# Performance work log

Hardware: AMD Instinct MI355X
Metric: run time of the kernel (lower is better)

The kernel has to match this reference:

```python
import jax, jax.numpy as jnp
import numpy as np

B, C, L = 4, 512, 2048
CI = 512          # inter_channels (must equal num_heads*head_dim)
H, D = 8, 64      # num_heads, head_dim = C // H
EPS = 1e-5        # BatchNorm1d eps


def setup_inputs() -> dict:
    key = jax.random.key(0)
    ks = jax.random.split(key, 9)
    s_in = 1.0 / np.sqrt(C)
    s_ci = 1.0 / np.sqrt(CI)
    return {
        "x": jax.random.normal(ks[0], (B, C, L), dtype=jnp.float32),
        "g_w": jax.random.uniform(ks[1], (CI, C), jnp.float32, -s_in, s_in),
        "g_b": jax.random.uniform(ks[2], (CI,), jnp.float32, -s_in, s_in),
        "theta_w": jax.random.uniform(ks[3], (CI, C), jnp.float32, -s_in, s_in),
        "theta_b": jax.random.uniform(ks[4], (CI,), jnp.float32, -s_in, s_in),
        "phi_w": jax.random.uniform(ks[5], (CI, C), jnp.float32, -s_in, s_in),
        "phi_b": jax.random.uniform(ks[6], (CI,), jnp.float32, -s_in, s_in),
        "w_w": jax.random.uniform(ks[7], (C, CI), jnp.float32, -s_ci, s_ci),
        "w_b": jax.random.uniform(ks[8], (C,), jnp.float32, -s_ci, s_ci),
        # BN affine params (torch inits them to 0, which zeroes the output;
        # use random values so the reference output / grads are non-trivial)
        "bn_gamma": jax.random.normal(jax.random.fold_in(key, 10), (C,), jnp.float32),
        "bn_beta": jax.random.normal(jax.random.fold_in(key, 11), (C,), jnp.float32),
    }


def _conv1x1(w, b, x):
    # x: [B, Cin, L], w: [Cout, Cin] -> [B, Cout, L]
    return jnp.einsum("oc,bcl->bol", w, x) + b[None, :, None]


def reference(x, g_w, g_b, theta_w, theta_b, phi_w, phi_b, w_w, w_b, bn_gamma, bn_beta):
    b, _, l = x.shape
    # 1x1 conv projections, split into heads: [B, H, D, L]
    g_x = _conv1x1(g_w, g_b, x).reshape(b, H, D, l).transpose(0, 1, 3, 2)      # [B,H,L,D]
    theta_x = _conv1x1(theta_w, theta_b, x).reshape(b, H, D, l).transpose(0, 1, 3, 2)  # [B,H,L,D]
    phi_x = _conv1x1(phi_w, phi_b, x).reshape(b, H, D, l)                       # [B,H,D,L]

    scale = 1.0 / jnp.sqrt(jnp.asarray(D, dtype=x.dtype))
    scores = jnp.einsum("bhqd,bhdk->bhqk", theta_x, phi_x) * scale  # [B,H,L,L]
    attn = jax.nn.softmax(scores, axis=-1)
    y = jnp.einsum("bhqk,bhkd->bhqd", attn, g_x)                    # [B,H,L,D]
    y = y.transpose(0, 1, 3, 2).reshape(b, CI, l)                   # [B,CI,L]

    # W: 1x1 conv + BatchNorm1d (training mode, biased batch stats)
    wy = _conv1x1(w_w, w_b, y)                                      # [B,C,L]
    mean = jnp.mean(wy, axis=(0, 2), keepdims=True)
    var = jnp.mean((wy - mean) ** 2, axis=(0, 2), keepdims=True)
    wy_hat = (wy - mean) * jax.lax.rsqrt(var + EPS)
    return wy_hat * bn_gamma[None, :, None] + bn_beta[None, :, None]
```

## Files before the change

### kernel.cpp

```cpp
#include <hip/hip_runtime.h>

constexpr int Bn = 4, Cn = 512, Ln = 2048, CIn = 512, Hn = 8, Dn = 64;
constexpr int COn = 3 * CIn;

typedef unsigned short u16;
typedef unsigned int u32;
typedef __attribute__((ext_vector_type(8))) short bfrag;
typedef __attribute__((ext_vector_type(4))) float facc;

#define SCF 0.180336879f

__device__ __forceinline__ facc mfma16(bfrag a, bfrag b, facc c) {
  return __builtin_amdgcn_mfma_f32_16x16x32_bf16(a, b, c, 0, 0, 0);
}

__device__ __forceinline__ void async16(const void* g, void* l) {
  __builtin_amdgcn_global_load_lds((const __attribute__((address_space(1))) void*)g,
                                   (__attribute__((address_space(3))) void*)l, 16, 0, 0);
}

__device__ __forceinline__ u16 f2bf(float x) {
  union { float f; u32 u; } v; v.f = x;
  u32 r = v.u + 0x7FFFu + ((v.u >> 16) & 1u);
  return (u16)(r >> 16);
}

__device__ __forceinline__ u16 f2bf_fast(float x) {
  union { float f; u32 u; } v; v.f = x;
  return (u16)((v.u + 0x8000u) >> 16);
}

__device__ __forceinline__ u32 pkbf(float lof, float hif) {
  union { float f; u32 u; } a, b; a.f = lof; b.f = hif;
  return __builtin_amdgcn_perm(b.u + 0x8000u, a.u + 0x8000u, 0x07060302u);
}

__device__ __forceinline__ bfrag fr8(const u16* base, int row, int gi) {
  return *(const bfrag*)&base[row * 64 + ((gi ^ (row & 7)) * 8)];
}

__global__ void k_wconv(const float* __restrict__ gw, const float* __restrict__ tw,
                        const float* __restrict__ pw, const float* __restrict__ ww,
                        u16* __restrict__ Wcat, u16* __restrict__ Ww,
                        float* __restrict__ stats) {
  int i = blockIdx.x * 256 + threadIdx.x;
  if (i < CIn * Cn) {
    Wcat[i]                = f2bf(tw[i] * SCF);
    Wcat[CIn * Cn + i]     = f2bf(pw[i]);
    Wcat[2 * CIn * Cn + i] = f2bf(gw[i]);
    Ww[i]                  = f2bf(ww[i]);
  }
  if (i < 2 * Cn) stats[i] = 0.f;
}

__global__ void k_xpose(const float* __restrict__ x, u16* __restrict__ xT) {
  __shared__ float tile[32][33];
  int b = blockIdx.z;
  int l0 = blockIdx.x * 32, c0 = blockIdx.y * 32;
  int tx = threadIdx.x & 31, ty = threadIdx.x >> 5;
  const float* xb = x + (size_t)b * Cn * Ln;
  for (int k = 0; k < 4; k++)
    tile[ty + k * 8][tx] = xb[(size_t)(c0 + ty + k * 8) * Ln + l0 + tx];
  __syncthreads();
  u16* xtb = xT + (size_t)b * Ln * Cn;
  int cc = (threadIdx.x & 15) * 2, r0 = threadIdx.x >> 4;
  for (int k = 0; k < 2; k++) {
    int ll = r0 + k * 16;
    u32 pk = pkbf(tile[cc][ll], tile[cc + 1][ll]);
    *(u32*)&xtb[(size_t)(l0 + ll) * Cn + c0 + cc] = pk;
  }
}

__device__ __forceinline__ void stage128x32(const u16* g, int K, int k0, u16* lds,
                                            int w, int l) {
  int gsw = ((l & 3) ^ ((l >> 3) & 3)) * 8;
  for (int jj = 0; jj < 2; jj++) {
    int j = w * 2 + jj;
    const u16* ga = g + (size_t)(j * 16 + (l >> 2)) * K + k0 + gsw;
    async16(ga, (char*)lds + j * 1024 + l * 16);
  }
}

__device__ __forceinline__ void gemm_core(const u16* A, const u16* Bt, int K,
                                          u16* As, u16* Bs, facc acc[4][4],
                                          int w, int l) {
  int quad = l >> 4, lo = l & 15;
  int mw = (w >> 1) * 64, nw = (w & 1) * 64;
  int rsw = (lo >> 1) & 3;
  for (int k0 = 0; k0 < K; k0 += 32) {
    stage128x32(A, K, k0, As, w, l);
    stage128x32(Bt, K, k0, Bs, w, l);
    __syncthreads();
    bfrag af[4], bfv[4];
    for (int mi = 0; mi < 4; mi++)
      af[mi] = *(const bfrag*)&As[(mw + mi * 16 + lo) * 32 + ((quad ^ rsw) * 8)];
    for (int ni = 0; ni < 4; ni++)
      bfv[ni] = *(const bfrag*)&Bs[(nw + ni * 16 + lo) * 32 + ((quad ^ rsw) * 8)];
    for (int mi = 0; mi < 4; mi++)
      for (int ni = 0; ni < 4; ni++)
        acc[mi][ni] = mfma16(af[mi], bfv[ni], acc[mi][ni]);
    __syncthreads();
  }
}

__global__ __launch_bounds__(256) void k_proj(
    const u16* __restrict__ Wcat, const u16* __restrict__ xT,
    const float* __restrict__ tb, const float* __restrict__ pb,
    const float* __restrict__ gb, u16* __restrict__ Q, u16* __restrict__ Kb,
    u16* __restrict__ Vt) {
  __shared__ __align__(16) u16 As[128 * 32];
  __shared__ __align__(16) u16 Bs[128 * 32];
  int w = threadIdx.x >> 6, l = threadIdx.x & 63;
  int quad = l >> 4, lo = l & 15;
  int m0 = blockIdx.y * 128, n0 = blockIdx.x * 128, b = blockIdx.z;
  facc acc[4][4] = {};
  gemm_core(Wcat + (size_t)m0 * Cn, xT + ((size_t)b * Ln + n0) * Cn, Cn, As, Bs, acc, w, l);
  int mw = (w >> 1) * 64, nw = (w & 1) * 64;
  int chunk = m0 >> 9;
  for (int mi = 0; mi < 4; mi++) {
    int mo = (m0 + mw + mi * 16) & 511;
    int hh = mo >> 6;
    int db = (mo & 63) + quad * 4;
    int bi = mo + quad * 4;
    if (chunk < 2) {
      const float* bias = (chunk == 0) ? tb : pb;
      float bs = (chunk == 0) ? SCF : 1.0f;
      u16* dst0 = ((chunk == 0) ? Q : Kb) + (size_t)(b * Hn + hh) * Ln * 64 + db;
      float b0 = bias[bi] * bs, b1 = bias[bi + 1] * bs;
      float b2 = bias[bi + 2] * bs, b3 = bias[bi + 3] * bs;
      for (int ni = 0; ni < 4; ni++) {
        int lcol = n0 + nw + ni * 16 + lo;
        facc a = acc[mi][ni];
        uint2 pk;
        pk.x = pkbf(a[0] + b0, a[1] + b1);
        pk.y = pkbf(a[2] + b2, a[3] + b3);
        *(uint2*)(dst0 + (size_t)lcol * 64) = pk;
      }
    } else {
      for (int ni = 0; ni < 4; ni++) {
        int lcol = n0 + nw + ni * 16 + lo;
        facc a = acc[mi][ni];
        for (int r = 0; r < 4; r++)
          Vt[((size_t)(b * Hn + hh) * Dn + db + r) * Ln + lcol] = f2bf_fast(a[r] + gb[bi + r]);
      }
    }
  }
}

__global__ __launch_bounds__(256, 2) void k_attn(
    const u16* __restrict__ Q, const u16* __restrict__ Kb,
    const u16* __restrict__ Vt, u16* __restrict__ yT) {
  __shared__ __align__(16) u16 lds[24576];
  u16* Ks = lds;
  u16* Vs = lds + 8192;
  u16* QPs = lds + 16384;
  int w = threadIdx.x >> 6, l = threadIdx.x & 63;
  int quad = l >> 4, lo = l & 15;
  int q0 = blockIdx.x * 128, h = blockIdx.y, b = blockIdx.z;
  size_t bh = (size_t)b * Hn + h;
  const u16* Qg = Q + bh * Ln * 64;
  const u16* Kg = Kb + bh * Ln * 64;
  const u16* Vg = Vt + bh * (size_t)Dn * Ln;

  int rin = l >> 3;
  int gg = ((l & 7) ^ rin) * 8;

  for (int jj = 0; jj < 4; jj++) {
    int j = w * 4 + jj;
    async16(Qg + (size_t)(q0 + j * 8 + rin) * 64 + gg, (char*)QPs + j * 1024 + l * 16);
  }
  for (int jj = 0; jj < 2; jj++) {
    int j = w * 2 + jj;
    async16(Kg + (size_t)(j * 8 + rin) * 64 + gg, (char*)Ks + j * 1024 + l * 16);
    async16(Vg + (size_t)(j * 8 + rin) * Ln + gg, (char*)Vs + j * 1024 + l * 16);
  }
  __syncthreads();
  bfrag qf[2][2];
  for (int s = 0; s < 2; s++)
    for (int c = 0; c < 2; c++)
      qf[s][c] = fr8(QPs, w * 32 + s * 16 + lo, c * 4 + quad);

  facc o[2][4] = {};
  float l_i[2] = {0.f, 0.f};

  for (int t = 0; t < 32; t++) {
    const u16* Kc = Ks + (t & 1) * 4096;
    const u16* Vc = Vs + (t & 1) * 4096;
    if (t < 31) {
      int nb = (~t & 1) * 4096;
      int kbase = (t + 1) * 64;
      for (int jj = 0; jj < 2; jj++) {
        int j = w * 2 + jj;
        async16(Kg + (size_t)(kbase + j * 8 + rin) * 64 + gg,
                (char*)(Ks + nb) + j * 1024 + l * 16);
        async16(Vg + (size_t)(j * 8 + rin) * Ln + kbase + gg,
                (char*)(Vs + nb) + j * 1024 + l * 16);
      }
    }
    for (int ni = 0; ni < 4; ni++) {
      bfrag kf0 = fr8(Kc, ni * 16 + lo, quad);
      bfrag kf1 = fr8(Kc, ni * 16 + lo, 4 + quad);
      for (int s = 0; s < 2; s++) {
        facc z = {};
        facc stv = mfma16(kf1, qf[s][1], mfma16(kf0, qf[s][0], z));
        float p0 = __builtin_amdgcn_exp2f(stv[0]);
        float p1 = __builtin_amdgcn_exp2f(stv[1]);
        float p2 = __builtin_amdgcn_exp2f(stv[2]);
        float p3 = __builtin_amdgcn_exp2f(stv[3]);
        l_i[s] += (p0 + p1) + (p2 + p3);
        int row = w * 32 + s * 16 + lo;
        uint2 pk;
        pk.x = pkbf(p0, p1);
        pk.y = pkbf(p2, p3);
        int gi = ni * 2 + (quad >> 1);
        *(uint2*)&QPs[row * 64 + ((gi ^ (row & 7)) * 8) + (quad & 1) * 4] = pk;
      }
    }
    bfrag pb2[2][2];
    for (int s = 0; s < 2; s++)
      for (int c = 0; c < 2; c++)
        pb2[s][c] = fr8(QPs, w * 32 + s * 16 + lo, c * 4 + quad);
    for (int mi = 0; mi < 4; mi++) {
      bfrag vf0 = fr8(Vc, mi * 16 + lo, quad);
      bfrag vf1 = fr8(Vc, mi * 16 + lo, 4 + quad);
      for (int s = 0; s < 2; s++)
        o[s][mi] = mfma16(vf1, pb2[s][1], mfma16(vf0, pb2[s][0], o[s][mi]));
    }
    __syncthreads();
  }
  for (int s = 0; s < 2; s++) {
    float lt = l_i[s];
    lt += __shfl_xor(lt, 16);
    lt += __shfl_xor(lt, 32);
    float inv = 1.0f / lt;
    int q = q0 + w * 32 + s * 16 + lo;
    u16* dst = yT + ((size_t)b * Ln + q) * CIn + h * 64;
    for (int mi = 0; mi < 4; mi++) {
      uint2 pk;
      pk.x = pkbf(o[s][mi][0] * inv, o[s][mi][1] * inv);
      pk.y = pkbf(o[s][mi][2] * inv, o[s][mi][3] * inv);
      *(uint2*)(dst + mi * 16 + quad * 4) = pk;
    }
  }
}

__global__ __launch_bounds__(256) void k_wgemm(
    const u16* __restrict__ Ww, const u16* __restrict__ yT,
    const float* __restrict__ wb, u16* __restrict__ wy,
    float* __restrict__ stats) {
  __shared__ __align__(16) u16 As[128 * 32];
  __shared__ __align__(16) u16 Bs[128 * 32];
  int w = threadIdx.x >> 6, l = threadIdx.x & 63;
  int quad = l >> 4, lo = l & 15;
  int m0 = blockIdx.y * 128, n0 = blockIdx.x * 128, b = blockIdx.z;
  facc acc[4][4] = {};
  gemm_core(Ww + (size_t)m0 * CIn, yT + ((size_t)b * Ln + n0) * CIn, CIn, As, Bs, acc, w, l);
  int mw = (w >> 1) * 64, nw = (w & 1) * 64;
  for (int mi = 0; mi < 4; mi++) {
    int cb = m0 + mw + mi * 16 + quad * 4;
    for (int r = 0; r < 4; r++) {
      float bias = wb[cb + r];
      float s = 0.f, q = 0.f;
      for (int ni = 0; ni < 4; ni++) {
        float v = acc[mi][ni][r] + bias;
        wy[((size_t)b * Cn + cb + r) * Ln + n0 + nw + ni * 16 + lo] = f2bf_fast(v);
        s += v; q += v * v;
      }
      for (int mask = 1; mask < 16; mask <<= 1) {
        s += __shfl_xor(s, mask);
        q += __shfl_xor(q, mask);
      }
      if (lo == 0) {
        atomicAdd(&stats[cb + r], s);
        atomicAdd(&stats[Cn + cb + r], q);
      }
    }
  }
}

__global__ void k_bn(const u16* __restrict__ wy, const float* __restrict__ stats,
                     const float* __restrict__ gam, const float* __restrict__ bet,
                     float* __restrict__ out) {
  int i = blockIdx.x * 256 + threadIdx.x;
  size_t idx = (size_t)i * 8;
  int c = (int)((idx >> 11) & (Cn - 1));
  const float invN = 1.f / (Bn * Ln);
  float mean = stats[c] * invN;
  float var = stats[Cn + c] * invN - mean * mean;
  float scl = gam[c] * rsqrtf(var + 1e-5f);
  float sh = bet[c] - mean * scl;
  uint4 v = *(const uint4*)(wy + idx);
  float4 o0, o1;
  o0.x = __uint_as_float((v.x & 0xFFFFu) << 16) * scl + sh;
  o0.y = __uint_as_float((v.x & 0xFFFF0000u)) * scl + sh;
  o0.z = __uint_as_float((v.y & 0xFFFFu) << 16) * scl + sh;
  o0.w = __uint_as_float((v.y & 0xFFFF0000u)) * scl + sh;
  o1.x = __uint_as_float((v.z & 0xFFFFu) << 16) * scl + sh;
  o1.y = __uint_as_float((v.z & 0xFFFF0000u)) * scl + sh;
  o1.z = __uint_as_float((v.w & 0xFFFFu) << 16) * scl + sh;
  o1.w = __uint_as_float((v.w & 0xFFFF0000u)) * scl + sh;
  *(float4*)(out + idx) = o0;
  *(float4*)(out + idx + 4) = o1;
}

extern "C" void kernel_launch(void* const* d_in, const int* in_sizes, int n_in,
                              void* d_out, int out_size, void* d_ws, size_t ws_size,
                              hipStream_t stream) {
  const float* x   = (const float*)d_in[0];
  const float* g_w = (const float*)d_in[1];
  const float* g_b = (const float*)d_in[2];
  const float* t_w = (const float*)d_in[3];
  const float* t_b = (const float*)d_in[4];
  const float* p_w = (const float*)d_in[5];
  const float* p_b = (const float*)d_in[6];
  const float* w_w = (const float*)d_in[7];
  const float* w_b = (const float*)d_in[8];
  const float* gam = (const float*)d_in[9];
  const float* bet = (const float*)d_in[10];
  float* out = (float*)d_out;

  char* ws = (char*)d_ws;
  size_t off = 0;
  auto alloc = [&](size_t bytes) {
    char* p = ws + off; off += (bytes + 255) & ~(size_t)255; return p;
  };
  u16*  xT   = (u16*)alloc((size_t)Bn * Ln * Cn * 2);
  u16*  Wcat = (u16*)alloc((size_t)COn * Cn * 2);
  u16*  Ww   = (u16*)alloc((size_t)Cn * CIn * 2);
  u16*  Qb   = (u16*)alloc((size_t)Bn * Hn * Ln * Dn * 2);
  u16*  Kb   = (u16*)alloc((size_t)Bn * Hn * Ln * Dn * 2);
  u16*  Vt   = (u16*)alloc((size_t)Bn * Hn * Dn * Ln * 2);
  u16*  yT   = (u16*)alloc((size_t)Bn * Ln * CIn * 2);
  u16*  wy   = (u16*)alloc((size_t)Bn * Cn * Ln * 2);
  float* st  = (float*)alloc(2 * Cn * 4);
  if (ws_size < off) return;

  k_wconv<<<dim3(1024), 256, 0, stream>>>(g_w, t_w, p_w, w_w, Wcat, Ww, st);
  k_xpose<<<dim3(64, 16, 4), 256, 0, stream>>>(x, xT);
  k_proj<<<dim3(16, 12, 4), 256, 0, stream>>>(Wcat, xT, t_b, p_b, g_b, Qb, Kb, Vt);
  k_attn<<<dim3(16, 8, 4), 256, 0, stream>>>(Qb, Kb, Vt, yT);
  k_wgemm<<<dim3(16, 4, 4), 256, 0, stream>>>(Ww, yT, w_b, wy, st);
  k_bn<<<dim3(2048), 256, 0, stream>>>(wy, st, gam, bet, out);
}
```

Before: 204.3 us.

## Split attention over key halves, shrink W-GEMM tiles, merge prep kernels

The attention kernel now splits the key/value range into two halves per query tile. Each half writes unnormalised partial outputs and row sums, and a new combine kernel adds them and normalises into yT. This doubles the attention grid and shortens each block's serial key loop. The W-conv GEMM moves to 64-row tiles to double its block count, and the weight-conversion and transpose kernels are merged into one launch. The cost is an extra kernel, a round-trip of the partial outputs through memory, and bf16 rounding of the partials before they are combined.

Measured after the change: 195.5 us. 1.04x faster.

```diff
diff --git a/kernel.cpp b/kernel.cpp
--- a/kernel.cpp
+++ b/kernel.cpp
@@ -35,27 +35,31 @@
   return __builtin_amdgcn_perm(b.u + 0x8000u, a.u + 0x8000u, 0x07060302u);
 }
 
+__device__ __forceinline__ float bflo(u32 u) { return __uint_as_float(u << 16); }
+__device__ __forceinline__ float bfhi(u32 u) { return __uint_as_float(u & 0xFFFF0000u); }
+
 __device__ __forceinline__ bfrag fr8(const u16* base, int row, int gi) {
   return *(const bfrag*)&base[row * 64 + ((gi ^ (row & 7)) * 8)];
 }
 
-__global__ void k_wconv(const float* __restrict__ gw, const float* __restrict__ tw,
-                        const float* __restrict__ pw, const float* __restrict__ ww,
-                        u16* __restrict__ Wcat, u16* __restrict__ Ww,
-                        float* __restrict__ stats) {
-  int i = blockIdx.x * 256 + threadIdx.x;
-  if (i < CIn * Cn) {
-    Wcat[i]                = f2bf(tw[i] * SCF);
-    Wcat[CIn * Cn + i]     = f2bf(pw[i]);
-    Wcat[2 * CIn * Cn + i] = f2bf(gw[i]);
-    Ww[i]                  = f2bf(ww[i]);
-  }
-  if (i < 2 * Cn) stats[i] = 0.f;
-}
-
-__global__ void k_xpose(const float* __restrict__ x, u16* __restrict__ xT) {
+__global__ void k_misc(const float* __restrict__ x, const float* __restrict__ gw,
+                       const float* __restrict__ tw, const float* __restrict__ pw,
+                       const float* __restrict__ ww, u16* __restrict__ xT,
+                       u16* __restrict__ Wcat, u16* __restrict__ Ww,
+                       float* __restrict__ stats) {
+  int b = blockIdx.z;
+  if (b == 4) {
+    int i = (blockIdx.y * 64 + blockIdx.x) * 256 + threadIdx.x;
+    if (i < CIn * Cn) {
+      Wcat[i]                = f2bf(tw[i] * SCF);
+      Wcat[CIn * Cn + i]     = f2bf(pw[i]);
+      Wcat[2 * CIn * Cn + i] = f2bf(gw[i]);
+      Ww[i]                  = f2bf(ww[i]);
+    }
+    if (i < 2 * Cn) stats[i] = 0.f;
+    return;
+  }
   __shared__ float tile[32][33];
-  int b = blockIdx.z;
   int l0 = blockIdx.x * 32, c0 = blockIdx.y * 32;
   int tx = threadIdx.x & 31, ty = threadIdx.x >> 5;
   const float* xb = x + (size_t)b * Cn * Ln;
@@ -97,6 +101,29 @@
     for (int ni = 0; ni < 4; ni++)
       bfv[ni] = *(const bfrag*)&Bs[(nw + ni * 16 + lo) * 32 + ((quad ^ rsw) * 8)];
     for (int mi = 0; mi < 4; mi++)
+      for (int ni = 0; ni < 4; ni++)
+        acc[mi][ni] = mfma16(af[mi], bfv[ni], acc[mi][ni]);
+    __syncthreads();
+  }
+}
+
+__device__ __forceinline__ void gemm_core64(const u16* A, const u16* Bt, int K,
+                                            u16* As, u16* Bs, facc acc[2][4],
+                                            int w, int l) {
+  int quad = l >> 4, lo = l & 15;
+  int mw = (w >> 1) * 32, nw = (w & 1) * 64;
+  int rsw = (lo >> 1) & 3;
+  int gsw = ((l & 3) ^ ((l >> 3) & 3)) * 8;
+  for (int k0 = 0; k0 < K; k0 += 32) {
+    async16(A + (size_t)(w * 16 + (l >> 2)) * K + k0 + gsw, (char*)As + w * 1024 + l * 16);
+    stage128x32(Bt, K, k0, Bs, w, l);
+    __syncthreads();
+    bfrag af[2], bfv[4];
+    for (int mi = 0; mi < 2; mi++)
+      af[mi] = *(const bfrag*)&As[(mw + mi * 16 + lo) * 32 + ((quad ^ rsw) * 8)];
+    for (int ni = 0; ni < 4; ni++)
+      bfv[ni] = *(const bfrag*)&Bs[(nw + ni * 16 + lo) * 32 + ((quad ^ rsw) * 8)];
+    for (int mi = 0; mi < 2; mi++)
       for (int ni = 0; ni < 4; ni++)
         acc[mi][ni] = mfma16(af[mi], bfv[ni], acc[mi][ni]);
     __syncthreads();
@@ -149,18 +176,19 @@
 
 __global__ __launch_bounds__(256, 2) void k_attn(
     const u16* __restrict__ Q, const u16* __restrict__ Kb,
-    const u16* __restrict__ Vt, u16* __restrict__ yT) {
+    const u16* __restrict__ Vt, u16* __restrict__ Opart,
+    float* __restrict__ lpart) {
   __shared__ __align__(16) u16 lds[24576];
   u16* Ks = lds;
   u16* Vs = lds + 8192;
   u16* QPs = lds + 16384;
   int w = threadIdx.x >> 6, l = threadIdx.x & 63;
   int quad = l >> 4, lo = l & 15;
-  int q0 = blockIdx.x * 128, h = blockIdx.y, b = blockIdx.z;
+  int q0 = blockIdx.x * 128, h = blockIdx.y >> 1, split = blockIdx.y & 1, b = blockIdx.z;
   size_t bh = (size_t)b * Hn + h;
   const u16* Qg = Q + bh * Ln * 64;
-  const u16* Kg = Kb + bh * Ln * 64;
-  const u16* Vg = Vt + bh * (size_t)Dn * Ln;
+  const u16* Kg = Kb + bh * Ln * 64 + (size_t)split * 1024 * 64;
+  const u16* Vg = Vt + bh * (size_t)Dn * Ln + split * 1024;
 
   int rin = l >> 3;
   int gg = ((l & 7) ^ rin) * 8;
@@ -183,10 +211,10 @@
   facc o[2][4] = {};
   float l_i[2] = {0.f, 0.f};
 
-  for (int t = 0; t < 32; t++) {
+  for (int t = 0; t < 16; t++) {
     const u16* Kc = Ks + (t & 1) * 4096;
     const u16* Vc = Vs + (t & 1) * 4096;
-    if (t < 31) {
+    if (t < 15) {
       int nb = (~t & 1) * 4096;
       int kbase = (t + 1) * 64;
       for (int jj = 0; jj < 2; jj++) {
@@ -228,35 +256,54 @@
     }
     __syncthreads();
   }
+  int sb = split * 32 + (int)bh;
   for (int s = 0; s < 2; s++) {
     float lt = l_i[s];
     lt += __shfl_xor(lt, 16);
     lt += __shfl_xor(lt, 32);
-    float inv = 1.0f / lt;
     int q = q0 + w * 32 + s * 16 + lo;
-    u16* dst = yT + ((size_t)b * Ln + q) * CIn + h * 64;
+    u16* dst = Opart + ((size_t)sb * Ln + q) * 64;
     for (int mi = 0; mi < 4; mi++) {
       uint2 pk;
-      pk.x = pkbf(o[s][mi][0] * inv, o[s][mi][1] * inv);
-      pk.y = pkbf(o[s][mi][2] * inv, o[s][mi][3] * inv);
+      pk.x = pkbf(o[s][mi][0], o[s][mi][1]);
+      pk.y = pkbf(o[s][mi][2], o[s][mi][3]);
       *(uint2*)(dst + mi * 16 + quad * 4) = pk;
     }
-  }
+    if (quad == 0) lpart[(size_t)sb * Ln + q] = lt;
+  }
+}
+
+__global__ void k_comb(const u16* __restrict__ Opart, const float* __restrict__ lpart,
+                       u16* __restrict__ yT) {
+  int i = blockIdx.x * 256 + threadIdx.x;
+  int bhq = i >> 3, d0 = (i & 7) * 8;
+  int bh = bhq >> 11, q = bhq & 2047;
+  const u16* o1 = Opart + ((size_t)bh * Ln + q) * 64 + d0;
+  const u16* o2 = o1 + (size_t)32 * Ln * 64;
+  float inv = 1.0f / (lpart[bhq] + lpart[65536 + bhq]);
+  uint4 a = *(const uint4*)o1, c = *(const uint4*)o2;
+  uint4 r;
+  r.x = pkbf((bflo(a.x) + bflo(c.x)) * inv, (bfhi(a.x) + bfhi(c.x)) * inv);
+  r.y = pkbf((bflo(a.y) + bflo(c.y)) * inv, (bfhi(a.y) + bfhi(c.y)) * inv);
+  r.z = pkbf((bflo(a.z) + bflo(c.z)) * inv, (bfhi(a.z) + bfhi(c.z)) * inv);
+  r.w = pkbf((bflo(a.w) + bflo(c.w)) * inv, (bfhi(a.w) + bfhi(c.w)) * inv);
+  int b = bh >> 3, h = bh & 7;
+  *(uint4*)(yT + ((size_t)b * Ln + q) * CIn + h * 64 + d0) = r;
 }
 
 __global__ __launch_bounds__(256) void k_wgemm(
     const u16* __restrict__ Ww, const u16* __restrict__ yT,
     const float* __restrict__ wb, u16* __restrict__ wy,
     float* __restrict__ stats) {
-  __shared__ __align__(16) u16 As[128 * 32];
+  __shared__ __align__(16) u16 As[64 * 32];
   __shared__ __align__(16) u16 Bs[128 * 32];
   int w = threadIdx.x >> 6, l = threadIdx.x & 63;
   int quad = l >> 4, lo = l & 15;
-  int m0 = blockIdx.y * 128, n0 = blockIdx.x * 128, b = blockIdx.z;
-  facc acc[4][4] = {};
-  gemm_core(Ww + (size_t)m0 * CIn, yT + ((size_t)b * Ln + n0) * CIn, CIn, As, Bs, acc, w, l);
-  int mw = (w >> 1) * 64, nw = (w & 1) * 64;
-  for (int mi = 0; mi < 4; mi++) {
+  int m0 = blockIdx.y * 64, n0 = blockIdx.x * 128, b = blockIdx.z;
+  facc acc[2][4] = {};
+  gemm_core64(Ww + (size_t)m0 * CIn, yT + ((size_t)b * Ln + n0) * CIn, CIn, As, Bs, acc, w, l);
+  int mw = (w >> 1) * 32, nw = (w & 1) * 64;
+  for (int mi = 0; mi < 2; mi++) {
     int cb = m0 + mw + mi * 16 + quad * 4;
     for (int r = 0; r < 4; r++) {
       float bias = wb[cb + r];
@@ -291,14 +338,10 @@
   float sh = bet[c] - mean * scl;
   uint4 v = *(const uint4*)(wy + idx);
   float4 o0, o1;
-  o0.x = __uint_as_float((v.x & 0xFFFFu) << 16) * scl + sh;
-  o0.y = __uint_as_float((v.x & 0xFFFF0000u)) * scl + sh;
-  o0.z = __uint_as_float((v.y & 0xFFFFu) << 16) * scl + sh;
-  o0.w = __uint_as_float((v.y & 0xFFFF0000u)) * scl + sh;
-  o1.x = __uint_as_float((v.z & 0xFFFFu) << 16) * scl + sh;
-  o1.y = __uint_as_float((v.z & 0xFFFF0000u)) * scl + sh;
-  o1.z = __uint_as_float((v.w & 0xFFFFu) << 16) * scl + sh;
-  o1.w = __uint_as_float((v.w & 0xFFFF0000u)) * scl + sh;
+  o0.x = bflo(v.x) * scl + sh; o0.y = bfhi(v.x) * scl + sh;
+  o0.z = bflo(v.y) * scl + sh; o0.w = bfhi(v.y) * scl + sh;
+  o1.x = bflo(v.z) * scl + sh; o1.y = bfhi(v.z) * scl + sh;
+  o1.z = bflo(v.w) * scl + sh; o1.w = bfhi(v.w) * scl + sh;
   *(float4*)(out + idx) = o0;
   *(float4*)(out + idx + 4) = o1;
 }
@@ -331,14 +374,17 @@
   u16*  Kb   = (u16*)alloc((size_t)Bn * Hn * Ln * Dn * 2);
   u16*  Vt   = (u16*)alloc((size_t)Bn * Hn * Dn * Ln * 2);
   u16*  yT   = (u16*)alloc((size_t)Bn * Ln * CIn * 2);
-  u16*  wy   = (u16*)alloc((size_t)Bn * Cn * Ln * 2);
+  size_t opart_bytes = (size_t)2 * 32 * Ln * 64 * 2;
+  u16*  Opart = (u16*)alloc(opart_bytes);
+  u16*  wy    = Opart;
+  float* lpart = (float*)alloc((size_t)2 * 32 * Ln * 4);
   float* st  = (float*)alloc(2 * Cn * 4);
   if (ws_size < off) return;
 
-  k_wconv<<<dim3(1024), 256, 0, stream>>>(g_w, t_w, p_w, w_w, Wcat, Ww, st);
-  k_xpose<<<dim3(64, 16, 4), 256, 0, stream>>>(x, xT);
+  k_misc<<<dim3(64, 16, 5), 256, 0, stream>>>(x, g_w, t_w, p_w, w_w, xT, Wcat, Ww, st);
   k_proj<<<dim3(16, 12, 4), 256, 0, stream>>>(Wcat, xT, t_b, p_b, g_b, Qb, Kb, Vt);
-  k_attn<<<dim3(16, 8, 4), 256, 0, stream>>>(Qb, Kb, Vt, yT);
-  k_wgemm<<<dim3(16, 4, 4), 256, 0, stream>>>(Ww, yT, w_b, wy, st);
+  k_attn<<<dim3(16, 16, 4), 256, 0, stream>>>(Qb, Kb, Vt, Opart, lpart);
+  k_comb<<<dim3(2048), 256, 0, stream>>>(Opart, lpart, yT);
+  k_wgemm<<<dim3(16, 8, 4), 256, 0, stream>>>(Ww, yT, w_b, wy, st);
   k_bn<<<dim3(2048), 256, 0, stream>>>(wy, st, gam, bet, out);
 }
```
